# Kernel optimization log

Measured on AMD Instinct MI355X. Metric: run time of the kernel, lower is better.

## Reference

```python
import jax, jax.numpy as jnp
import numpy as np

B, T, D, U = 64, 2048, 256, 256

def hard_sigmoid(x):
    return jnp.clip(0.2 * x + 0.5, 0.0, 1.0)

def setup_inputs() -> dict:
    key = jax.random.key(0)
    k1, k2, k3 = jax.random.split(key, 3)
    x = jax.random.normal(k1, (B, T, D), dtype=jnp.float32)
    kernel = jax.random.normal(k2, (D, 3 * U), dtype=jnp.float32) * (1.0 / np.sqrt(D))
    recurrent_kernel = jax.random.normal(k3, (U, 3 * U), dtype=jnp.float32) * (1.0 / np.sqrt(U))
    bias = jnp.zeros((3 * U,), dtype=jnp.float32)
    return {"x": x, "kernel": kernel, "recurrent_kernel": recurrent_kernel, "bias": bias}

def reference(x, kernel, recurrent_kernel, bias):
    # implementation=0 style: precompute input projections for all timesteps in one big matmul
    # x: [B,T,D], kernel: [D,3U] -> xz/xr/xh each [B,T,U]
    units = recurrent_kernel.shape[0]
    x_proj = jnp.einsum('btd,dh->bth', x, kernel) + bias  # [B,T,3U]
    xz, xr, xh = jnp.split(x_proj, 3, axis=-1)
    Uz = recurrent_kernel[:, :units]
    Ur = recurrent_kernel[:, units:2 * units]
    Uh = recurrent_kernel[:, 2 * units:]

    def step(h, xs):
        xz_t, xr_t, xh_t = xs  # each [B,U]
        z = hard_sigmoid(xz_t + h @ Uz)
        r = hard_sigmoid(xr_t + h @ Ur)
        hh = jnp.tanh(xh_t + (r * h) @ Uh)
        h_new = z * h + (1.0 - z) * hh
        return h_new, None

    h0 = jnp.zeros((x.shape[0], units), dtype=x.dtype)
    # scan over time: move T to leading axis
    xs = (jnp.swapaxes(xz, 0, 1), jnp.swapaxes(xr, 0, 1), jnp.swapaxes(xh, 0, 1))
    h_last, _ = jax.lax.scan(step, h0, xs)
    return h_last  # [B, U] (return_sequences=False)
```

## Files before the change

### kernel.cpp

```cpp
#include <hip/hip_runtime.h>


#define TB 2048
#define NU 256
#define G3 768

typedef __attribute__((ext_vector_type(8))) short bf16x8;
typedef __attribute__((ext_vector_type(4))) float f32x4;

__device__ inline unsigned short f2bf(float f){
  union{float f; unsigned u;} v; v.f = f;
  unsigned r = v.u + 0x7fffu + ((v.u >> 16) & 1u);
  return (unsigned short)(r >> 16);
}
__device__ inline unsigned pk2(float a, float b){
  return (unsigned)f2bf(a) | ((unsigned)f2bf(b) << 16);
}
__device__ inline float bflo(unsigned u){
  union{unsigned u; float f;} v; v.u = u << 16; return v.f;
}
__device__ inline float bfhi(unsigned u){
  union{unsigned u; float f;} v; v.u = u & 0xffff0000u; return v.f;
}
__device__ inline unsigned cvtpk(float a, float b){
  unsigned r;
  asm("v_cvt_pk_bf16_f32 %0, %1, %2" : "=v"(r) : "v"(a), "v"(b));
  return r;
}
__device__ inline float exp2_fast(float x){
#if __has_builtin(__builtin_amdgcn_exp2f)
  return __builtin_amdgcn_exp2f(x);
#else
  float r; asm("v_exp_f32 %0, %1" : "=v"(r) : "v"(x)); return r;
#endif
}

__global__ __launch_bounds__(256) void transpose_k(const float* __restrict__ W,
                                                   const float* __restrict__ R,
                                                   unsigned short* __restrict__ Wt,
                                                   unsigned short* __restrict__ Ut){
  int n = blockIdx.x;
  int k = threadIdx.x;
  if (n < G3) Wt[n*NU + k] = f2bf(W[k*G3 + n]);
  else        Ut[(n-G3)*NU + k] = f2bf(R[k*G3 + (n-G3)]);
}

__global__ __launch_bounds__(256) void proj_k(const float* __restrict__ x,
                                              const unsigned short* __restrict__ Wt,
                                              const float* __restrict__ bias,
                                              unsigned short* __restrict__ XA,
                                              unsigned short* __restrict__ XB){
  __shared__ short As[4096];
  __shared__ short Bs[4096];
  __shared__ short St[4096];
  const int tid  = threadIdx.x;
  const int lane = tid & 63;
  const int wv   = tid >> 6;
  const int wr   = wv >> 1, wc = wv & 1;
  const int q    = lane >> 4, r16 = lane & 15;
  const int tm   = blockIdx.x;
  const int bn   = blockIdx.y;

  f32x4 acc[2][2];
  #pragma unroll
  for (int a=0;a<2;a++)
    #pragma unroll
    for (int b=0;b<2;b++) acc[a][b] = {0.f,0.f,0.f,0.f};

  const int mA = tid >> 2, kq = tid & 3;
  const int kc32 = kq >> 1, q0 = (kq & 1) * 2;

  for (int kc0 = 0; kc0 < 256; kc0 += 64){
    {
      const float* src = x + (size_t)mA*(2048*256) + (size_t)tm*256 + kc0 + kq*16;
      float4 f0 = *(const float4*)(src);
      float4 f1 = *(const float4*)(src+4);
      float4 f2 = *(const float4*)(src+8);
      float4 f3 = *(const float4*)(src+12);
      *(uint2*)&As[kc32*2048 + q0*512     + mA*8 + 0] = make_uint2(pk2(f0.x,f0.y), pk2(f0.z,f0.w));
      *(uint2*)&As[kc32*2048 + q0*512     + mA*8 + 4] = make_uint2(pk2(f1.x,f1.y), pk2(f1.z,f1.w));
      *(uint2*)&As[kc32*2048 + (q0+1)*512 + mA*8 + 0] = make_uint2(pk2(f2.x,f2.y), pk2(f2.z,f2.w));
      *(uint2*)&As[kc32*2048 + (q0+1)*512 + mA*8 + 4] = make_uint2(pk2(f3.x,f3.y), pk2(f3.z,f3.w));
    }
    {
      const unsigned short* srcB = Wt + (size_t)(bn*64 + mA)*256 + kc0 + kq*16;
      uint4 b0v = *(const uint4*)(srcB);
      uint4 b1v = *(const uint4*)(srcB+8);
      *(uint4*)&Bs[kc32*2048 + q0*512     + mA*8] = b0v;
      *(uint4*)&Bs[kc32*2048 + (q0+1)*512 + mA*8] = b1v;
    }
    __syncthreads();
    #pragma unroll
    for (int kk = 0; kk < 2; kk++){
      bf16x8 av[2], bv[2];
      #pragma unroll
      for (int rt=0; rt<2; rt++)
        av[rt] = *(const bf16x8*)&As[kk*2048 + q*512 + (wr*32+rt*16+r16)*8];
      #pragma unroll
      for (int ct=0; ct<2; ct++)
        bv[ct] = *(const bf16x8*)&Bs[kk*2048 + q*512 + (wc*32+ct*16+r16)*8];
      #pragma unroll
      for (int rt=0; rt<2; rt++)
        #pragma unroll
        for (int ct=0; ct<2; ct++)
          acc[rt][ct] = __builtin_amdgcn_mfma_f32_16x16x32_bf16(av[rt], bv[ct], acc[rt][ct], 0,0,0);
    }
    __syncthreads();
  }

  const int csub = (bn < 4) ? 0 : (bn < 8 ? 256 : 512);
  #pragma unroll
  for (int rt=0; rt<2; rt++){
    #pragma unroll
    for (int ct=0; ct<2; ct++){
      int colg = bn*64 + wc*32 + ct*16 + r16;
      float bb = bias[colg];
      int c = colg - csub;
      int wi = (c >> 5) & 1, tt2 = (c >> 4) & 1, r16g = c & 15;
      #pragma unroll
      for (int i=0;i<4;i++){
        int b = wr*32 + rt*16 + q*4 + i;
        int gg = b >> 4, lb = b & 15;
        int lane_ = (lb >> 2)*16 + r16g, ii = lb & 3;
        St[(gg*2+wi)*512 + lane_*8 + tt2*4 + ii] = (short)f2bf(acc[rt][ct][i] + bb);
      }
    }
  }
  __syncthreads();

  #pragma unroll
  for (int it=0; it<2; it++){
    int idx = tid + it*256;
    int chunk = idx >> 6, within = idx & 63;
    int gg = chunk >> 1, wi = chunk & 1;
    int w_ = (bn & 3)*2 + wi;
    uint4 val = *(const uint4*)&St[chunk*512 + within*8];
    if (bn < 8){
      int sel = (bn < 4) ? 0 : 1;
      *((uint4*)XA + ((((size_t)tm*4+gg)*8 + w_)*64 + within)*2 + sel) = val;
    } else {
      *((uint4*)XB + (((size_t)tm*4+gg)*8 + w_)*64 + within) = val;
    }
  }
}

__global__ __launch_bounds__(512, 2) void gru_k(const unsigned short* __restrict__ XA,
                                                const unsigned short* __restrict__ XB,
                                                const unsigned short* __restrict__ Ut,
                                                float* __restrict__ out){
  __shared__ short fb[8192];

  const int tid  = threadIdx.x;
  const int w    = tid >> 6;
  const int lane = tid & 63;
  const int q    = lane >> 4, r16 = lane & 15;
  const int g    = blockIdx.x;
  const int b0   = g * 16;

  for (int i = tid; i < 8192; i += 512) fb[i] = 0;

  bf16x8 Uz[2][8], Ur[2][8], Uh[2][8];
  #pragma unroll
  for (int tt=0; tt<2; tt++){
    int cz = w*32 + tt*16 + r16;
    #pragma unroll
    for (int kc=0; kc<8; kc++){
      Uz[tt][kc] = *(const bf16x8*)&Ut[(cz      )*256 + kc*32 + q*8];
      Ur[tt][kc] = *(const bf16x8*)&Ut[(cz + 256)*256 + kc*32 + q*8];
      Uh[tt][kc] = *(const bf16x8*)&Ut[(cz + 512)*256 + kc*32 + q*8];
    }
  }

  float hprev[2][4] = {{0.f,0.f,0.f,0.f},{0.f,0.f,0.f,0.f}};
  float z8[2][4];

  const int wbase = w*512 + (r16>>3)*128 + q*32 + (r16&7);

  const uint4* pA = (const uint4*)XA + ((size_t)(g*8+w)*64 + lane)*2;
  const uint4* pB = (const uint4*)XB + ((size_t)(g*8+w)*64 + lane);

  uint4 xa0 = pA[0], xa1 = pA[1];
  uint4 xb0 = pB[0];
  pA += 4096; pB += 2048;

  __syncthreads();

  #pragma unroll 1
  for (int t = 0; t < TB; t++){
    uint4 na0 = pA[0], na1 = pA[1];
    uint4 nb0 = pB[0];
    pA += 4096; pB += 2048;

    unsigned xw[8] = {xa0.x,xa0.y,xa0.z,xa0.w,xa1.x,xa1.y,xa1.z,xa1.w};

    f32x4 az[2], ar[2];
    #pragma unroll
    for (int tt=0; tt<2; tt++){
      #pragma unroll
      for (int i=0;i<4;i++){
        int s  = tt*4 + i;
        int sr = 8 + s;
        az[tt][i] = (s&1)  ? bfhi(xw[s>>1])  : bflo(xw[s>>1]);
        ar[tt][i] = (sr&1) ? bfhi(xw[sr>>1]) : bflo(xw[sr>>1]);
      }
    }
    #pragma unroll
    for (int kc=0; kc<8; kc++){
      bf16x8 a = *(const bf16x8*)&fb[kc*512 + lane*8];
      az[0] = __builtin_amdgcn_mfma_f32_16x16x32_bf16(a, Uz[0][kc], az[0], 0,0,0);
      az[1] = __builtin_amdgcn_mfma_f32_16x16x32_bf16(a, Uz[1][kc], az[1], 0,0,0);
      ar[0] = __builtin_amdgcn_mfma_f32_16x16x32_bf16(a, Ur[0][kc], ar[0], 0,0,0);
      ar[1] = __builtin_amdgcn_mfma_f32_16x16x32_bf16(a, Ur[1][kc], ar[1], 0,0,0);
    }
    #pragma unroll
    for (int tt=0; tt<2; tt++){
      #pragma unroll
      for (int i=0;i<4;i++){
        float rr = __builtin_amdgcn_fmed3f(fmaf(0.2f, ar[tt][i], 0.5f), 0.f, 1.f);
        float v  = rr * hprev[tt][i];
        fb[4096 + wbase + tt*256 + i*8] = (short)cvtpk(v, v);
      }
    }
    #pragma unroll
    for (int tt=0; tt<2; tt++)
      #pragma unroll
      for (int i=0;i<4;i++)
        z8[tt][i] = __builtin_amdgcn_fmed3f(fmaf(0.2f, az[tt][i], 0.5f), 0.f, 1.f);
    __syncthreads();

    f32x4 ah[2];
    {
      unsigned xwb[4] = {xb0.x,xb0.y,xb0.z,xb0.w};
      #pragma unroll
      for (int ct=0; ct<2; ct++){
        #pragma unroll
        for (int i=0;i<4;i++){
          int s = ct*4 + i;
          ah[ct][i] = (s&1) ? bfhi(xwb[s>>1]) : bflo(xwb[s>>1]);
        }
      }
    }
    #pragma unroll
    for (int kc=0; kc<8; kc++){
      bf16x8 a = *(const bf16x8*)&fb[4096 + kc*512 + lane*8];
      ah[0] = __builtin_amdgcn_mfma_f32_16x16x32_bf16(a, Uh[0][kc], ah[0], 0,0,0);
      ah[1] = __builtin_amdgcn_mfma_f32_16x16x32_bf16(a, Uh[1][kc], ah[1], 0,0,0);
    }
    #pragma unroll
    for (int ct=0; ct<2; ct++){
      #pragma unroll
      for (int i=0;i<4;i++){
        float e  = exp2_fast(2.8853900817779268f * ah[ct][i]);
        float rc = __builtin_amdgcn_rcpf(e + 1.f);
        float hh = fmaf(-2.f, rc, 1.f);
        float hn = fmaf(z8[ct][i], hprev[ct][i] - hh, hh);
        hprev[ct][i] = hn;
        fb[wbase + ct*256 + i*8] = (short)cvtpk(hn, hn);
      }
    }
    __syncthreads();

    xa0 = na0; xa1 = na1; xb0 = nb0;
  }

  #pragma unroll
  for (int ct=0; ct<2; ct++)
    #pragma unroll
    for (int i=0;i<4;i++)
      out[(size_t)(b0 + q*4 + i)*256 + w*32 + ct*16 + r16] = hprev[ct][i];
}

extern "C" void kernel_launch(void* const* d_in, const int* in_sizes, int n_in,
                              void* d_out, int out_size, void* d_ws, size_t ws_size,
                              hipStream_t stream) {
  (void)in_sizes; (void)n_in; (void)out_size; (void)ws_size;
  const float* x    = (const float*)d_in[0];
  const float* Wk   = (const float*)d_in[1];
  const float* Rk   = (const float*)d_in[2];
  const float* bias = (const float*)d_in[3];
  float* out = (float*)d_out;

  unsigned short* XA = (unsigned short*)d_ws;
  unsigned short* XB = XA + (size_t)2048*32768;
  unsigned short* Wt = XB + (size_t)2048*16384;
  unsigned short* Ut = Wt + (size_t)768*256;

  hipLaunchKernelGGL(transpose_k, dim3(1536),    dim3(256), 0, stream, Wk, Rk, Wt, Ut);
  hipLaunchKernelGGL(proj_k,      dim3(2048,12), dim3(256), 0, stream, x, Wt, bias, XA, XB);
  hipLaunchKernelGGL(gru_k,       dim3(4),       dim3(512), 0, stream, XA, XB, Ut, out);
}
```

Measured before the change: 3.527 ms.

## Reorder GRU step to shorten critical path with double-buffered h and swizzled LDS

```diff
diff --git a/kernel.cpp b/kernel.cpp
--- a/kernel.cpp
+++ b/kernel.cpp
@@ -148,7 +148,7 @@
                                                 const unsigned short* __restrict__ XB,
                                                 const unsigned short* __restrict__ Ut,
                                                 float* __restrict__ out){
-  __shared__ short fb[8192];
+  __shared__ short fb[12288];
 
   const int tid  = threadIdx.x;
   const int w    = tid >> 6;
@@ -157,7 +157,11 @@
   const int g    = blockIdx.x;
   const int b0   = g * 16;
 
-  for (int i = tid; i < 8192; i += 512) fb[i] = 0;
+  const int lswz = (lane & ~3) | ((lane & 3) ^ ((((lane >> 4) & 1) << 1) | ((lane >> 3) & 1)));
+  const int ix   = ((r16 >> 3) << 1) | ((lane >> 5) & 1);
+  const int wrb  = w*512 + (r16 >> 3)*128 + q*32 + (r16 & 7);
+
+  for (int i = tid; i < 12288; i += 512) fb[i] = 0;
 
   bf16x8 Uz[2][8], Ur[2][8], Uh[2][8];
   #pragma unroll
@@ -172,9 +176,6 @@
   }
 
   float hprev[2][4] = {{0.f,0.f,0.f,0.f},{0.f,0.f,0.f,0.f}};
-  float z8[2][4];
-
-  const int wbase = w*512 + (r16>>3)*128 + q*32 + (r16&7);
 
   const uint4* pA = (const uint4*)XA + ((size_t)(g*8+w)*64 + lane)*2;
   const uint4* pB = (const uint4*)XB + ((size_t)(g*8+w)*64 + lane);
@@ -191,71 +192,73 @@
     uint4 nb0 = pB[0];
     pA += 4096; pB += 2048;
 
-    unsigned xw[8] = {xa0.x,xa0.y,xa0.z,xa0.w,xa1.x,xa1.y,xa1.z,xa1.w};
-
-    f32x4 az[2], ar[2];
-    #pragma unroll
-    for (int tt=0; tt<2; tt++){
-      #pragma unroll
-      for (int i=0;i<4;i++){
-        int s  = tt*4 + i;
-        int sr = 8 + s;
-        az[tt][i] = (s&1)  ? bfhi(xw[s>>1])  : bflo(xw[s>>1]);
-        ar[tt][i] = (sr&1) ? bfhi(xw[sr>>1]) : bflo(xw[sr>>1]);
-      }
-    }
+    const int hb = (t & 1) ? 4096 : 0;
+
+    f32x4 ar[2];
+    {
+      unsigned xw1[4] = {xa1.x,xa1.y,xa1.z,xa1.w};
+      #pragma unroll
+      for (int tt=0; tt<2; tt++)
+        #pragma unroll
+        for (int i=0;i<4;i++){
+          int s = tt*4 + i;
+          ar[tt][i] = (s&1) ? bfhi(xw1[s>>1]) : bflo(xw1[s>>1]);
+        }
+    }
+    bf16x8 af[8];
+    __builtin_amdgcn_s_setprio(1);
     #pragma unroll
     for (int kc=0; kc<8; kc++){
-      bf16x8 a = *(const bf16x8*)&fb[kc*512 + lane*8];
-      az[0] = __builtin_amdgcn_mfma_f32_16x16x32_bf16(a, Uz[0][kc], az[0], 0,0,0);
-      az[1] = __builtin_amdgcn_mfma_f32_16x16x32_bf16(a, Uz[1][kc], az[1], 0,0,0);
-      ar[0] = __builtin_amdgcn_mfma_f32_16x16x32_bf16(a, Ur[0][kc], ar[0], 0,0,0);
-      ar[1] = __builtin_amdgcn_mfma_f32_16x16x32_bf16(a, Ur[1][kc], ar[1], 0,0,0);
-    }
+      af[kc] = *(const bf16x8*)&fb[hb + kc*512 + lswz*8];
+      ar[0] = __builtin_amdgcn_mfma_f32_16x16x32_bf16(af[kc], Ur[0][kc], ar[0], 0,0,0);
+      ar[1] = __builtin_amdgcn_mfma_f32_16x16x32_bf16(af[kc], Ur[1][kc], ar[1], 0,0,0);
+    }
+    __builtin_amdgcn_s_setprio(0);
     #pragma unroll
     for (int tt=0; tt<2; tt++){
       #pragma unroll
       for (int i=0;i<4;i++){
         float rr = __builtin_amdgcn_fmed3f(fmaf(0.2f, ar[tt][i], 0.5f), 0.f, 1.f);
         float v  = rr * hprev[tt][i];
-        fb[4096 + wbase + tt*256 + i*8] = (short)cvtpk(v, v);
+        fb[8192 + wrb + tt*256 + ((i^ix)<<3)] = (short)cvtpk(v, v);
       }
     }
-    #pragma unroll
-    for (int tt=0; tt<2; tt++)
-      #pragma unroll
-      for (int i=0;i<4;i++)
-        z8[tt][i] = __builtin_amdgcn_fmed3f(fmaf(0.2f, az[tt][i], 0.5f), 0.f, 1.f);
-    __syncthreads();
-
-    f32x4 ah[2];
-    {
+    __syncthreads();
+
+    f32x4 az[2], ah[2];
+    {
+      unsigned xw0[4] = {xa0.x,xa0.y,xa0.z,xa0.w};
       unsigned xwb[4] = {xb0.x,xb0.y,xb0.z,xb0.w};
       #pragma unroll
-      for (int ct=0; ct<2; ct++){
+      for (int tt=0; tt<2; tt++)
         #pragma unroll
         for (int i=0;i<4;i++){
-          int s = ct*4 + i;
-          ah[ct][i] = (s&1) ? bfhi(xwb[s>>1]) : bflo(xwb[s>>1]);
+          int s = tt*4 + i;
+          az[tt][i] = (s&1) ? bfhi(xw0[s>>1]) : bflo(xw0[s>>1]);
+          ah[tt][i] = (s&1) ? bfhi(xwb[s>>1]) : bflo(xwb[s>>1]);
         }
-      }
-    }
+    }
+    __builtin_amdgcn_s_setprio(1);
     #pragma unroll
     for (int kc=0; kc<8; kc++){
-      bf16x8 a = *(const bf16x8*)&fb[4096 + kc*512 + lane*8];
-      ah[0] = __builtin_amdgcn_mfma_f32_16x16x32_bf16(a, Uh[0][kc], ah[0], 0,0,0);
-      ah[1] = __builtin_amdgcn_mfma_f32_16x16x32_bf16(a, Uh[1][kc], ah[1], 0,0,0);
-    }
+      bf16x8 vv = *(const bf16x8*)&fb[8192 + kc*512 + lswz*8];
+      az[0] = __builtin_amdgcn_mfma_f32_16x16x32_bf16(af[kc], Uz[0][kc], az[0], 0,0,0);
+      az[1] = __builtin_amdgcn_mfma_f32_16x16x32_bf16(af[kc], Uz[1][kc], az[1], 0,0,0);
+      ah[0] = __builtin_amdgcn_mfma_f32_16x16x32_bf16(vv,     Uh[0][kc], ah[0], 0,0,0);
+      ah[1] = __builtin_amdgcn_mfma_f32_16x16x32_bf16(vv,     Uh[1][kc], ah[1], 0,0,0);
+    }
+    __builtin_amdgcn_s_setprio(0);
     #pragma unroll
     for (int ct=0; ct<2; ct++){
       #pragma unroll
       for (int i=0;i<4;i++){
+        float z = __builtin_amdgcn_fmed3f(fmaf(0.2f, az[ct][i], 0.5f), 0.f, 1.f);
         float e  = exp2_fast(2.8853900817779268f * ah[ct][i]);
         float rc = __builtin_amdgcn_rcpf(e + 1.f);
         float hh = fmaf(-2.f, rc, 1.f);
-        float hn = fmaf(z8[ct][i], hprev[ct][i] - hh, hh);
+        float hn = fmaf(z, hprev[ct][i] - hh, hh);
         hprev[ct][i] = hn;
-        fb[wbase + ct*256 + i*8] = (short)cvtpk(hn, hn);
+        fb[(hb^4096) + wrb + ct*256 + ((i^ix)<<3)] = (short)cvtpk(hn, hn);
       }
     }
     __syncthreads();
```

Measured after the change: 5.579 ms. +58.2%, slower.
